# Kernel optimization log

Measured on AMD Instinct MI355X. Metric: run time of the kernel, lower is better.

Reference implementation:

```python
import jax, jax.numpy as jnp
import numpy as np

D = 1024
E = 8


def setup_inputs() -> dict:
    key = jax.random.key(0)
    ks = jax.random.split(key, 7)
    s = 1.0 / np.sqrt(D)
    x = jax.random.normal(ks[0], (4, 2048, D), dtype=jnp.float32)
    Wg = jax.random.uniform(ks[1], (D, E), minval=-s, maxval=s, dtype=jnp.float32)
    bg = jax.random.uniform(ks[2], (E,), minval=-s, maxval=s, dtype=jnp.float32)
    W1 = jax.random.uniform(ks[3], (E, D, D), minval=-s, maxval=s, dtype=jnp.float32)
    b1 = jax.random.uniform(ks[4], (E, D), minval=-s, maxval=s, dtype=jnp.float32)
    W2 = jax.random.uniform(ks[5], (E, D, D), minval=-s, maxval=s, dtype=jnp.float32)
    b2 = jax.random.uniform(ks[6], (E, D), minval=-s, maxval=s, dtype=jnp.float32)
    return {"x": x, "Wg": Wg, "bg": bg, "W1": W1, "b1": b1, "W2": W2, "b2": b2}


def reference(x, Wg, bg, W1, b1, W2, b2):
    N, T, d = x.shape
    x_flat = x.reshape(N * T, d)                                  # [NT, D]
    logits = x_flat @ Wg + bg                                     # [NT, E]
    probs = jax.nn.softmax(logits, axis=-1)
    assignments = jnp.argmax(probs, axis=-1)                      # [NT]
    # all-experts MLP (dense, as in the original module)
    h = jnp.einsum('nd,edh->neh', x_flat, W1) + b1[None]          # [NT, E, D]
    h = jax.nn.gelu(h, approximate=False)                         # torch GELU = exact erf
    eo = jnp.einsum('neh,ehd->ned', h, W2) + b2[None]             # [NT, E, D]
    selected = jnp.take_along_axis(eo, assignments[:, None, None], axis=1)[:, 0, :]  # [NT, D]
    w = jnp.take_along_axis(probs, assignments[:, None], axis=1)  # [NT, 1]
    out = (w * selected).reshape(N, T, d)
    return out
```

## Files before the change

kernel.cpp:

```cpp
#include <hip/hip_runtime.h>
#include <cstdint>

#define NT 8192
#define DD 1024
#define NE 8
#define BK 32
#define NKIT (DD / BK)
#define MAXTILE 72

typedef __attribute__((ext_vector_type(8))) _Float16 half8;
typedef __attribute__((ext_vector_type(4))) float f32x4;

__device__ __forceinline__ unsigned short f2h_bits(float f) {
  _Float16 h = (_Float16)f;
  return __builtin_bit_cast(unsigned short, h);
}

#define GLDS16(gp, lp) __builtin_amdgcn_global_load_lds( \
  (__attribute__((address_space(1))) void*)(uintptr_t)(gp), \
  (__attribute__((address_space(3))) void*)(uintptr_t)(lp), 16, 0, 0)

#define WAITCNT_VM12 0xF7C
#define WAITCNT_VM8  0xF78
#define WAITCNT_VM4  0xF74
#define WAITCNT_VM0  0xF70

__global__ __launch_bounds__(256) void wcast_kernel(
    const float* __restrict__ W1, const float* __restrict__ W2,
    _Float16* __restrict__ W1t, _Float16* __restrict__ W2t) {
  __shared__ float tile[64][65];
  const int z = blockIdx.z;
  const float* W = (z < 8 ? W1 : W2) + (size_t)(z & 7) * (DD * DD);
  _Float16* Wt   = (z < 8 ? W1t : W2t) + (size_t)(z & 7) * (DD * DD);
  const int k0 = blockIdx.x * 64, n0 = blockIdx.y * 64;
  const int tid = threadIdx.x;
#pragma unroll
  for (int it = 0; it < 4; ++it) {
    int idx = it * 256 + tid;
    int r = idx >> 4;
    int q = idx & 15;
    float4 v = *(const float4*)(W + (size_t)(k0 + r) * DD + n0 + q * 4);
    tile[r][q * 4 + 0] = v.x; tile[r][q * 4 + 1] = v.y;
    tile[r][q * 4 + 2] = v.z; tile[r][q * 4 + 3] = v.w;
  }
  __syncthreads();
#pragma unroll
  for (int it = 0; it < 4; ++it) {
    int idx = it * 256 + tid;
    int n = idx >> 4;
    int q = idx & 15;
    ushort4 o;
    o.x = f2h_bits(tile[q * 4 + 0][n]);
    o.y = f2h_bits(tile[q * 4 + 1][n]);
    o.z = f2h_bits(tile[q * 4 + 2][n]);
    o.w = f2h_bits(tile[q * 4 + 3][n]);
    *(ushort4*)(Wt + (size_t)(n0 + n) * DD + k0 + q * 4) = o;
  }
}

__global__ __launch_bounds__(256) void gate_kernel(
    const float* __restrict__ x, const float* __restrict__ Wg, const float* __restrict__ bg,
    int* __restrict__ assign, float* __restrict__ wgt, _Float16* __restrict__ xh) {
  __shared__ float WgL[NE * DD];
  const int tid = threadIdx.x;
#pragma unroll
  for (int it = 0; it < 8; ++it) {
    int idx = it * 256 + tid;
    float4 v = ((const float4*)Wg)[idx];
    int k = idx >> 1;
    int e0 = (idx & 1) * 4;
    WgL[(e0 + 0) * DD + k] = v.x;
    WgL[(e0 + 1) * DD + k] = v.y;
    WgL[(e0 + 2) * DD + k] = v.z;
    WgL[(e0 + 3) * DD + k] = v.w;
  }
  __syncthreads();
  const int lane = tid & 63, w = tid >> 6;
#pragma unroll
  for (int s = 0; s < 2; ++s) {
    const int t = blockIdx.x * 8 + w * 2 + s;
    const float4* xr = (const float4*)(x + (size_t)t * DD);
    float4 xv[4];
#pragma unroll
    for (int c = 0; c < 4; ++c) xv[c] = xr[lane + 64 * c];
    ushort4* xo = (ushort4*)(xh + (size_t)t * DD);
#pragma unroll
    for (int c = 0; c < 4; ++c) {
      union { ushort4 u; _Float16 h[4]; } cv;
      cv.h[0] = (_Float16)xv[c].x; cv.h[1] = (_Float16)xv[c].y;
      cv.h[2] = (_Float16)xv[c].z; cv.h[3] = (_Float16)xv[c].w;
      xo[lane + 64 * c] = cv.u;
    }
    float p[NE];
#pragma unroll
    for (int e = 0; e < NE; ++e) {
      float acc = 0.f;
#pragma unroll
      for (int c = 0; c < 4; ++c) {
        float4 wv = *(const float4*)&WgL[e * DD + 4 * lane + 256 * c];
        acc += xv[c].x * wv.x + xv[c].y * wv.y + xv[c].z * wv.z + xv[c].w * wv.w;
      }
      p[e] = acc;
    }
#pragma unroll
    for (int e = 0; e < NE; ++e) {
      float v = p[e];
      for (int off = 32; off > 0; off >>= 1) v += __shfl_down(v, off, 64);
      p[e] = v;
    }
    if (lane == 0) {
      float l[NE];
#pragma unroll
      for (int e = 0; e < NE; ++e) l[e] = p[e] + bg[e];
      int a = 0; float best = l[0];
#pragma unroll
      for (int e = 1; e < NE; ++e) if (l[e] > best) { best = l[e]; a = e; }
      float sum = 0.f;
#pragma unroll
      for (int e = 0; e < NE; ++e) sum += expf(l[e] - best);
      assign[t] = a;
      wgt[t] = 1.0f / sum;
    }
  }
}

__global__ __launch_bounds__(1024) void sort_kernel(
    const int* __restrict__ assign, int* __restrict__ rowtok, int* __restrict__ plan) {
  __shared__ int sc[NE * 1024];
  const int tid = threadIdx.x;
  int a[8];
  int c[NE];
#pragma unroll
  for (int e = 0; e < NE; ++e) c[e] = 0;
#pragma unroll
  for (int j = 0; j < 8; ++j) { a[j] = assign[tid * 8 + j]; ++c[a[j]]; }
#pragma unroll
  for (int e = 0; e < NE; ++e) sc[e * 1024 + tid] = c[e];
  __syncthreads();
  for (int d = 1; d < 1024; d <<= 1) {
    int add[NE];
    if (tid >= d) {
#pragma unroll
      for (int e = 0; e < NE; ++e) add[e] = sc[e * 1024 + tid - d];
    }
    __syncthreads();
    if (tid >= d) {
#pragma unroll
      for (int e = 0; e < NE; ++e) sc[e * 1024 + tid] += add[e];
    }
    __syncthreads();
  }
  int tot[NE], incl[NE];
#pragma unroll
  for (int e = 0; e < NE; ++e) { tot[e] = sc[e * 1024 + 1023]; incl[e] = sc[e * 1024 + tid]; }
  int offs[NE];
  {
    int s = 0;
#pragma unroll
    for (int e = 0; e < NE; ++e) { offs[e] = s; s += tot[e]; }
  }
  int run[NE];
#pragma unroll
  for (int e = 0; e < NE; ++e) run[e] = offs[e] + incl[e] - c[e];
#pragma unroll
  for (int j = 0; j < 8; ++j) { int e = a[j]; rowtok[run[e]++] = tid * 8 + j; }
  if (tid == 0) {
    int nt = 0;
    for (int e = 0; e < NE; ++e) {
      int cc = tot[e], st = offs[e];
      int t_cnt = (cc + 127) >> 7;
      for (int t = 0; t < t_cnt; ++t) {
        plan[1 + nt] = e;
        plan[1 + MAXTILE + nt] = st + t * 128;
        plan[1 + 2 * MAXTILE + nt] = st + cc;
        ++nt;
      }
    }
    plan[0] = nt;
  }
}

template <int MODE>
__global__ __launch_bounds__(256) void gemm_kernel(
    const _Float16* __restrict__ A,
    const _Float16* __restrict__ Wt,
    const float* __restrict__ bias,
    const int* __restrict__ plan,
    _Float16* __restrict__ Hout,
    float* __restrict__ Fout,
    const int* __restrict__ rowtok,
    const float* __restrict__ wgt) {
  const int wrk = blockIdx.x;
  const int tile = wrk >> 3;
  if (tile >= plan[0]) return;
  const int e = plan[1 + tile];
  const int m0 = plan[1 + MAXTILE + tile];
  const int seg_end = plan[1 + 2 * MAXTILE + tile];
  const int n0 = (wrk & 7) * 128;

  const int tid = threadIdx.x;
  const int lane = tid & 63;
  const int w = tid >> 6;
  const int wm = w >> 1, wn = w & 1;
  const int quad = lane >> 4;
  const int r15 = lane & 15;

  __shared__ alignas(16) _Float16 As[4 * 128 * BK];
  __shared__ alignas(16) _Float16 Bs[4 * 128 * BK];
  char* ldsA = (char*)As;
  char* ldsB = (char*)Bs;

  const _Float16* We = Wt + (size_t)e * DD * DD;
  const _Float16* gAp[2];
  const _Float16* gBp[2];
  int ldso[2];
#pragma unroll
  for (int i = 0; i < 2; ++i) {
    int slot = i * 256 + tid;
    int row = slot >> 2;
    int c = (slot & 3) ^ ((row >> 1) & 3);
    int rg = m0 + row; if (rg > NT - 1) rg = NT - 1;
    int arow = (MODE == 0) ? rowtok[rg] : rg;
    gAp[i] = A + (size_t)arow * DD + c * 8;
    gBp[i] = We + (size_t)(n0 + row) * DD + c * 8;
    ldso[i] = slot * 16;
  }

  int aoff[4], boff[4];
#pragma unroll
  for (int i = 0; i < 4; ++i) {
    int m = wm * 64 + i * 16 + r15;
    aoff[i] = m * 4 + (quad ^ ((m >> 1) & 3));
    int n = wn * 64 + i * 16 + r15;
    boff[i] = n * 4 + (quad ^ ((n >> 1) & 3));
  }

  f32x4 acc[4][4];
  f32x4 zero4 = {0.f, 0.f, 0.f, 0.f};
#pragma unroll
  for (int mi = 0; mi < 4; ++mi)
#pragma unroll
    for (int ni = 0; ni < 4; ++ni) acc[mi][ni] = zero4;

#define STAGE(KT) do {                                               \
    const int b_ = (KT) & 3;                                         \
    char* la_ = ldsA + (b_ << 13);                                   \
    char* lb_ = ldsB + (b_ << 13);                                   \
    const int ko_ = (KT) * BK;                                       \
    _Pragma("unroll") for (int i_ = 0; i_ < 2; ++i_)                 \
      GLDS16(gAp[i_] + ko_, la_ + ldso[i_]);                         \
    _Pragma("unroll") for (int i_ = 0; i_ < 2; ++i_)                 \
      GLDS16(gBp[i_] + ko_, lb_ + ldso[i_]);                         \
  } while (0)

  STAGE(0); STAGE(1); STAGE(2);

#pragma unroll 1
  for (int kt = 0; kt < NKIT; ++kt) {
    __builtin_amdgcn_s_barrier();
    __asm__ volatile("" ::: "memory");
    if (kt + 3 < NKIT) STAGE(kt + 3);
    if (kt < NKIT - 3)      __builtin_amdgcn_s_waitcnt(WAITCNT_VM12);
    else if (kt == NKIT - 3) __builtin_amdgcn_s_waitcnt(WAITCNT_VM8);
    else if (kt == NKIT - 2) __builtin_amdgcn_s_waitcnt(WAITCNT_VM4);
    else                     __builtin_amdgcn_s_waitcnt(WAITCNT_VM0);
    __builtin_amdgcn_s_barrier();
    __asm__ volatile("" ::: "memory");
    const int buf = kt & 3;
    const half8* AsV = (const half8*)(ldsA + (buf << 13));
    const half8* BsV = (const half8*)(ldsB + (buf << 13));
    half8 a[4], b[4];
#pragma unroll
    for (int i = 0; i < 4; ++i) a[i] = AsV[aoff[i]];
#pragma unroll
    for (int i = 0; i < 4; ++i) b[i] = BsV[boff[i]];
#pragma unroll
    for (int mi = 0; mi < 4; ++mi)
#pragma unroll
      for (int ni = 0; ni < 4; ++ni)
        acc[mi][ni] = __builtin_amdgcn_mfma_f32_16x16x32_f16(a[mi], b[ni], acc[mi][ni], 0, 0, 0);
  }
#undef STAGE

  const float* bptr = bias + (size_t)e * DD;
  if (MODE == 0) {
#pragma unroll
    for (int mi = 0; mi < 4; ++mi) {
      int rowb = m0 + wm * 64 + mi * 16 + quad * 4;
#pragma unroll
      for (int r = 0; r < 4; ++r) {
        int gpos = rowb + r;
        if (gpos < seg_end) {
#pragma unroll
          for (int ni = 0; ni < 4; ++ni) {
            int n = n0 + wn * 64 + ni * 16 + r15;
            float val = acc[mi][ni][r] + bptr[n];
            val = 0.5f * val * (1.0f + erff(val * 0.70710678118654752f));
            Hout[(size_t)gpos * DD + n] = (_Float16)val;
          }
        }
      }
    }
  } else {
#pragma unroll
    for (int mi = 0; mi < 4; ++mi) {
      int rowb = m0 + wm * 64 + mi * 16 + quad * 4;
#pragma unroll
      for (int r = 0; r < 4; ++r) {
        int gpos = rowb + r;
        if (gpos < seg_end) {
          int tok = rowtok[gpos];
          float wv = wgt[tok];
          float* orow = Fout + (size_t)tok * DD;
#pragma unroll
          for (int ni = 0; ni < 4; ++ni) {
            int n = n0 + wn * 64 + ni * 16 + r15;
            orow[n] = (acc[mi][ni][r] + bptr[n]) * wv;
          }
        }
      }
    }
  }
}

extern "C" void kernel_launch(void* const* d_in, const int* in_sizes, int n_in,
                              void* d_out, int out_size, void* d_ws, size_t ws_size,
                              hipStream_t stream) {
  const float* x  = (const float*)d_in[0];
  const float* Wg = (const float*)d_in[1];
  const float* bg = (const float*)d_in[2];
  const float* W1 = (const float*)d_in[3];
  const float* b1 = (const float*)d_in[4];
  const float* W2 = (const float*)d_in[5];
  const float* b2 = (const float*)d_in[6];
  float* out = (float*)d_out;

  char* ws = (char*)d_ws;
  const size_t MB16 = (size_t)1 << 24;
  _Float16* W1t = (_Float16*)(ws + 0 * MB16);
  _Float16* W2t = (_Float16*)(ws + 1 * MB16);
  _Float16* xh  = (_Float16*)(ws + 2 * MB16);
  _Float16* H   = (_Float16*)(ws + 3 * MB16);
  int*   assign = (int*)(ws + 4 * MB16);
  int*   rowtok = assign + NT;
  float* wgt    = (float*)(rowtok + NT);
  int*   plan   = (int*)(wgt + NT);

  wcast_kernel<<<dim3(16, 16, 16), 256, 0, stream>>>(W1, W2, W1t, W2t);
  gate_kernel<<<NT / 8, 256, 0, stream>>>(x, Wg, bg, assign, wgt, xh);
  sort_kernel<<<1, 1024, 0, stream>>>(assign, rowtok, plan);
  gemm_kernel<0><<<MAXTILE * 8, 256, 0, stream>>>(xh, W1t, b1, plan, H, nullptr, rowtok, nullptr);
  gemm_kernel<1><<<MAXTILE * 8, 256, 0, stream>>>(H, W2t, b2, plan, nullptr, out, rowtok, wgt);
}
```

Measured before the change: 262.5 us.

## Split GEMM K dimension across two 256-thread pipes within a block

Doubles the GEMM block to 512 threads, with each half computing the partial product over half of the K range using its own double-buffered LDS stage. The two partial accumulators are then combined through a swizzled LDS buffer before the bias, GELU or weighting epilogue. The aim is more waves per tile and more latency hiding, since only about 72x8 tiles exist and they underfill the GPU. In exchange, pipeline depth drops from four stages to two, LDS use rises to 64KB, and an extra reduction pass plus barriers is added.

```diff
diff --git a/kernel.cpp b/kernel.cpp
--- a/kernel.cpp
+++ b/kernel.cpp
@@ -5,7 +5,8 @@
 #define DD 1024
 #define NE 8
 #define BK 32
-#define NKIT (DD / BK)
+#define KHALF 512
+#define NKIT2 (KHALF / BK)
 #define MAXTILE 72
 
 typedef __attribute__((ext_vector_type(8))) _Float16 half8;
@@ -20,8 +21,6 @@
   (__attribute__((address_space(1))) void*)(uintptr_t)(gp), \
   (__attribute__((address_space(3))) void*)(uintptr_t)(lp), 16, 0, 0)
 
-#define WAITCNT_VM12 0xF7C
-#define WAITCNT_VM8  0xF78
 #define WAITCNT_VM4  0xF74
 #define WAITCNT_VM0  0xF70
 
@@ -181,7 +180,7 @@
 }
 
 template <int MODE>
-__global__ __launch_bounds__(256) void gemm_kernel(
+__global__ __launch_bounds__(512) void gemm_kernel(
     const _Float16* __restrict__ A,
     const _Float16* __restrict__ Wt,
     const float* __restrict__ bias,
@@ -199,16 +198,19 @@
   const int n0 = (wrk & 7) * 128;
 
   const int tid = threadIdx.x;
+  const int pipe = tid >> 8;
+  const int ptid = tid & 255;
   const int lane = tid & 63;
   const int w = tid >> 6;
-  const int wm = w >> 1, wn = w & 1;
+  const int pw = w & 3;
+  const int wm = pw >> 1, wn = pw & 1;
   const int quad = lane >> 4;
   const int r15 = lane & 15;
-
-  __shared__ alignas(16) _Float16 As[4 * 128 * BK];
-  __shared__ alignas(16) _Float16 Bs[4 * 128 * BK];
-  char* ldsA = (char*)As;
-  char* ldsB = (char*)Bs;
+  const int kbase = pipe * KHALF;
+
+  __shared__ alignas(16) char lds[65536];
+  char* ldsA = lds;
+  char* ldsB = lds + 32768;
 
   const _Float16* We = Wt + (size_t)e * DD * DD;
   const _Float16* gAp[2];
@@ -216,13 +218,13 @@
   int ldso[2];
 #pragma unroll
   for (int i = 0; i < 2; ++i) {
-    int slot = i * 256 + tid;
+    int slot = i * 256 + ptid;
     int row = slot >> 2;
     int c = (slot & 3) ^ ((row >> 1) & 3);
     int rg = m0 + row; if (rg > NT - 1) rg = NT - 1;
     int arow = (MODE == 0) ? rowtok[rg] : rg;
-    gAp[i] = A + (size_t)arow * DD + c * 8;
-    gBp[i] = We + (size_t)(n0 + row) * DD + c * 8;
+    gAp[i] = A + (size_t)arow * DD + kbase + c * 8;
+    gBp[i] = We + (size_t)(n0 + row) * DD + kbase + c * 8;
     ldso[i] = slot * 16;
   }
 
@@ -242,10 +244,10 @@
 #pragma unroll
     for (int ni = 0; ni < 4; ++ni) acc[mi][ni] = zero4;
 
-#define STAGE(KT) do {                                               \
-    const int b_ = (KT) & 3;                                         \
-    char* la_ = ldsA + (b_ << 13);                                   \
-    char* lb_ = ldsB + (b_ << 13);                                   \
+#define STAGE(KT, BUF) do {                                          \
+    const int rb_ = ((pipe << 1) | (BUF)) << 13;                     \
+    char* la_ = ldsA + rb_;                                          \
+    char* lb_ = ldsB + rb_;                                          \
     const int ko_ = (KT) * BK;                                       \
     _Pragma("unroll") for (int i_ = 0; i_ < 2; ++i_)                 \
       GLDS16(gAp[i_] + ko_, la_ + ldso[i_]);                         \
@@ -253,22 +255,23 @@
       GLDS16(gBp[i_] + ko_, lb_ + ldso[i_]);                         \
   } while (0)
 
-  STAGE(0); STAGE(1); STAGE(2);
+  STAGE(0, 0);
 
 #pragma unroll 1
-  for (int kt = 0; kt < NKIT; ++kt) {
+  for (int kt = 0; kt < NKIT2; ++kt) {
+    const int buf = kt & 1;
     __builtin_amdgcn_s_barrier();
     __asm__ volatile("" ::: "memory");
-    if (kt + 3 < NKIT) STAGE(kt + 3);
-    if (kt < NKIT - 3)      __builtin_amdgcn_s_waitcnt(WAITCNT_VM12);
-    else if (kt == NKIT - 3) __builtin_amdgcn_s_waitcnt(WAITCNT_VM8);
-    else if (kt == NKIT - 2) __builtin_amdgcn_s_waitcnt(WAITCNT_VM4);
-    else                     __builtin_amdgcn_s_waitcnt(WAITCNT_VM0);
+    if (kt + 1 < NKIT2) {
+      STAGE(kt + 1, buf ^ 1);
+      __builtin_amdgcn_s_waitcnt(WAITCNT_VM4);
+    } else {
+      __builtin_amdgcn_s_waitcnt(WAITCNT_VM0);
+    }
     __builtin_amdgcn_s_barrier();
     __asm__ volatile("" ::: "memory");
-    const int buf = kt & 3;
-    const half8* AsV = (const half8*)(ldsA + (buf << 13));
-    const half8* BsV = (const half8*)(ldsB + (buf << 13));
+    const half8* AsV = (const half8*)(ldsA + (((pipe << 1) | buf) << 13));
+    const half8* BsV = (const half8*)(ldsB + (((pipe << 1) | buf) << 13));
     half8 a[4], b[4];
 #pragma unroll
     for (int i = 0; i < 4; ++i) a[i] = AsV[aoff[i]];
@@ -282,40 +285,52 @@
   }
 #undef STAGE
 
+  __syncthreads();
+  float* comb = (float*)lds;
+  if (pipe == 1) {
+#pragma unroll
+    for (int mi = 0; mi < 4; ++mi) {
+      int rowb = wm * 64 + mi * 16 + quad * 4;
+#pragma unroll
+      for (int ni = 0; ni < 4; ++ni) {
+        int col = wn * 64 + ni * 16 + r15;
+        int cx = col ^ (quad << 4);
+#pragma unroll
+        for (int r = 0; r < 4; ++r) comb[(rowb + r) * 128 + cx] = acc[mi][ni][r];
+      }
+    }
+  }
+  __syncthreads();
+  if (pipe == 1) return;
+
   const float* bptr = bias + (size_t)e * DD;
-  if (MODE == 0) {
-#pragma unroll
-    for (int mi = 0; mi < 4; ++mi) {
-      int rowb = m0 + wm * 64 + mi * 16 + quad * 4;
-#pragma unroll
-      for (int r = 0; r < 4; ++r) {
-        int gpos = rowb + r;
-        if (gpos < seg_end) {
+#pragma unroll
+  for (int mi = 0; mi < 4; ++mi) {
+    int rowb = m0 + wm * 64 + mi * 16 + quad * 4;
+    int rowl = wm * 64 + mi * 16 + quad * 4;
+#pragma unroll
+    for (int r = 0; r < 4; ++r) {
+      int gpos = rowb + r;
+      if (gpos < seg_end) {
+        if (MODE == 0) {
 #pragma unroll
           for (int ni = 0; ni < 4; ++ni) {
-            int n = n0 + wn * 64 + ni * 16 + r15;
-            float val = acc[mi][ni][r] + bptr[n];
+            int col = wn * 64 + ni * 16 + r15;
+            int n = n0 + col;
+            float val = acc[mi][ni][r] + comb[(rowl + r) * 128 + (col ^ (quad << 4))] + bptr[n];
             val = 0.5f * val * (1.0f + erff(val * 0.70710678118654752f));
             Hout[(size_t)gpos * DD + n] = (_Float16)val;
           }
-        }
-      }
-    }
-  } else {
-#pragma unroll
-    for (int mi = 0; mi < 4; ++mi) {
-      int rowb = m0 + wm * 64 + mi * 16 + quad * 4;
-#pragma unroll
-      for (int r = 0; r < 4; ++r) {
-        int gpos = rowb + r;
-        if (gpos < seg_end) {
+        } else {
           int tok = rowtok[gpos];
           float wv = wgt[tok];
           float* orow = Fout + (size_t)tok * DD;
 #pragma unroll
           for (int ni = 0; ni < 4; ++ni) {
-            int n = n0 + wn * 64 + ni * 16 + r15;
-            orow[n] = (acc[mi][ni][r] + bptr[n]) * wv;
+            int col = wn * 64 + ni * 16 + r15;
+            int n = n0 + col;
+            float val = acc[mi][ni][r] + comb[(rowl + r) * 128 + (col ^ (quad << 4))] + bptr[n];
+            orow[n] = val * wv;
           }
         }
       }
@@ -349,6 +364,6 @@
   wcast_kernel<<<dim3(16, 16, 16), 256, 0, stream>>>(W1, W2, W1t, W2t);
   gate_kernel<<<NT / 8, 256, 0, stream>>>(x, Wg, bg, assign, wgt, xh);
   sort_kernel<<<1, 1024, 0, stream>>>(assign, rowtok, plan);
-  gemm_kernel<0><<<MAXTILE * 8, 256, 0, stream>>>(xh, W1t, b1, plan, H, nullptr, rowtok, nullptr);
-  gemm_kernel<1><<<MAXTILE * 8, 256, 0, stream>>>(H, W2t, b2, plan, nullptr, out, rowtok, wgt);
-}
+  gemm_kernel<0><<<MAXTILE * 8, 512, 0, stream>>>(xh, W1t, b1, plan, H, nullptr, rowtok, nullptr);
+  gemm_kernel<1><<<MAXTILE * 8, 512, 0, stream>>>(H, W2t, b2, plan, nullptr, out, rowtok, wgt);
+}
```

Result: no change. 263.7 us (+0.4%).

## Shrink GEMM tile to 64x128 and switch to double-buffered LDS pipeline

Applied to the files above, without the earlier changes.

Grouped expert GEMM tiles change from 128x128 to 64x128 rows, with each of the four waves covering all 64 rows and a 32-column slice. MAXTILE is raised to match. The 4-stage global-to-LDS prefetch becomes a 2-stage double buffer, cutting LDS from 64KB to 24KB. This aims to reduce padding waste on partially filled expert segments, launch more blocks, and raise occupancy. The cost is less arithmetic per loaded byte and a shallower prefetch that may hide memory latency less well. The launch grid must also be sized for the larger tile count, and that code is not visible here.

```diff
diff --git a/kernel.cpp b/kernel.cpp
--- a/kernel.cpp
+++ b/kernel.cpp
@@ -6,7 +6,8 @@
 #define NE 8
 #define BK 32
 #define NKIT (DD / BK)
-#define MAXTILE 72
+#define TM 64
+#define MAXTILE 136
 
 typedef __attribute__((ext_vector_type(8))) _Float16 half8;
 typedef __attribute__((ext_vector_type(4))) float f32x4;
@@ -20,9 +21,7 @@
   (__attribute__((address_space(1))) void*)(uintptr_t)(gp), \
   (__attribute__((address_space(3))) void*)(uintptr_t)(lp), 16, 0, 0)
 
-#define WAITCNT_VM12 0xF7C
-#define WAITCNT_VM8  0xF78
-#define WAITCNT_VM4  0xF74
+#define WAITCNT_VM3  0xF73
 #define WAITCNT_VM0  0xF70
 
 __global__ __launch_bounds__(256) void wcast_kernel(
@@ -168,10 +167,10 @@
     int nt = 0;
     for (int e = 0; e < NE; ++e) {
       int cc = tot[e], st = offs[e];
-      int t_cnt = (cc + 127) >> 7;
+      int t_cnt = (cc + TM - 1) / TM;
       for (int t = 0; t < t_cnt; ++t) {
         plan[1 + nt] = e;
-        plan[1 + MAXTILE + nt] = st + t * 128;
+        plan[1 + MAXTILE + nt] = st + t * TM;
         plan[1 + 2 * MAXTILE + nt] = st + cc;
         ++nt;
       }
@@ -200,121 +199,117 @@
 
   const int tid = threadIdx.x;
   const int lane = tid & 63;
-  const int w = tid >> 6;
-  const int wm = w >> 1, wn = w & 1;
+  const int wn = tid >> 6;
   const int quad = lane >> 4;
   const int r15 = lane & 15;
 
-  __shared__ alignas(16) _Float16 As[4 * 128 * BK];
-  __shared__ alignas(16) _Float16 Bs[4 * 128 * BK];
-  char* ldsA = (char*)As;
-  char* ldsB = (char*)Bs;
+  __shared__ alignas(16) char lds[24576];
+  char* ldsA = lds;
+  char* ldsB = lds + 8192;
 
   const _Float16* We = Wt + (size_t)e * DD * DD;
-  const _Float16* gAp[2];
+  const _Float16* gAp;
   const _Float16* gBp[2];
-  int ldso[2];
+  int ldsoA, ldsoB[2];
+  {
+    int slot = tid;
+    int row = slot >> 2;
+    int c = (slot & 3) ^ ((row >> 1) & 3);
+    int rg = m0 + row; if (rg > NT - 1) rg = NT - 1;
+    int arow = (MODE == 0) ? rowtok[rg] : rg;
+    gAp = A + (size_t)arow * DD + c * 8;
+    ldsoA = slot * 16;
+  }
 #pragma unroll
   for (int i = 0; i < 2; ++i) {
     int slot = i * 256 + tid;
     int row = slot >> 2;
     int c = (slot & 3) ^ ((row >> 1) & 3);
-    int rg = m0 + row; if (rg > NT - 1) rg = NT - 1;
-    int arow = (MODE == 0) ? rowtok[rg] : rg;
-    gAp[i] = A + (size_t)arow * DD + c * 8;
     gBp[i] = We + (size_t)(n0 + row) * DD + c * 8;
-    ldso[i] = slot * 16;
-  }
-
-  int aoff[4], boff[4];
+    ldsoB[i] = slot * 16;
+  }
+
+  int aoff[4], boff[2];
 #pragma unroll
   for (int i = 0; i < 4; ++i) {
-    int m = wm * 64 + i * 16 + r15;
+    int m = i * 16 + r15;
     aoff[i] = m * 4 + (quad ^ ((m >> 1) & 3));
-    int n = wn * 64 + i * 16 + r15;
+  }
+#pragma unroll
+  for (int i = 0; i < 2; ++i) {
+    int n = wn * 32 + i * 16 + r15;
     boff[i] = n * 4 + (quad ^ ((n >> 1) & 3));
   }
 
-  f32x4 acc[4][4];
+  f32x4 acc[4][2];
   f32x4 zero4 = {0.f, 0.f, 0.f, 0.f};
 #pragma unroll
   for (int mi = 0; mi < 4; ++mi)
 #pragma unroll
-    for (int ni = 0; ni < 4; ++ni) acc[mi][ni] = zero4;
-
-#define STAGE(KT) do {                                               \
-    const int b_ = (KT) & 3;                                         \
-    char* la_ = ldsA + (b_ << 13);                                   \
-    char* lb_ = ldsB + (b_ << 13);                                   \
+    for (int ni = 0; ni < 2; ++ni) acc[mi][ni] = zero4;
+
+#define STAGE(KT, BUF) do {                                          \
     const int ko_ = (KT) * BK;                                       \
-    _Pragma("unroll") for (int i_ = 0; i_ < 2; ++i_)                 \
-      GLDS16(gAp[i_] + ko_, la_ + ldso[i_]);                         \
-    _Pragma("unroll") for (int i_ = 0; i_ < 2; ++i_)                 \
-      GLDS16(gBp[i_] + ko_, lb_ + ldso[i_]);                         \
+    char* la_ = ldsA + ((BUF) << 12);                                \
+    char* lb_ = ldsB + ((BUF) << 13);                                \
+    GLDS16(gAp + ko_, la_ + ldsoA);                                  \
+    GLDS16(gBp[0] + ko_, lb_ + ldsoB[0]);                            \
+    GLDS16(gBp[1] + ko_, lb_ + ldsoB[1]);                            \
   } while (0)
 
-  STAGE(0); STAGE(1); STAGE(2);
+  STAGE(0, 0);
 
 #pragma unroll 1
   for (int kt = 0; kt < NKIT; ++kt) {
+    const int buf = kt & 1;
     __builtin_amdgcn_s_barrier();
     __asm__ volatile("" ::: "memory");
-    if (kt + 3 < NKIT) STAGE(kt + 3);
-    if (kt < NKIT - 3)      __builtin_amdgcn_s_waitcnt(WAITCNT_VM12);
-    else if (kt == NKIT - 3) __builtin_amdgcn_s_waitcnt(WAITCNT_VM8);
-    else if (kt == NKIT - 2) __builtin_amdgcn_s_waitcnt(WAITCNT_VM4);
-    else                     __builtin_amdgcn_s_waitcnt(WAITCNT_VM0);
+    if (kt + 1 < NKIT) {
+      STAGE(kt + 1, buf ^ 1);
+      __builtin_amdgcn_s_waitcnt(WAITCNT_VM3);
+    } else {
+      __builtin_amdgcn_s_waitcnt(WAITCNT_VM0);
+    }
     __builtin_amdgcn_s_barrier();
     __asm__ volatile("" ::: "memory");
-    const int buf = kt & 3;
-    const half8* AsV = (const half8*)(ldsA + (buf << 13));
+    const half8* AsV = (const half8*)(ldsA + (buf << 12));
     const half8* BsV = (const half8*)(ldsB + (buf << 13));
-    half8 a[4], b[4];
+    half8 a[4], b[2];
 #pragma unroll
     for (int i = 0; i < 4; ++i) a[i] = AsV[aoff[i]];
 #pragma unroll
-    for (int i = 0; i < 4; ++i) b[i] = BsV[boff[i]];
+    for (int i = 0; i < 2; ++i) b[i] = BsV[boff[i]];
 #pragma unroll
     for (int mi = 0; mi < 4; ++mi)
 #pragma unroll
-      for (int ni = 0; ni < 4; ++ni)
+      for (int ni = 0; ni < 2; ++ni)
         acc[mi][ni] = __builtin_amdgcn_mfma_f32_16x16x32_f16(a[mi], b[ni], acc[mi][ni], 0, 0, 0);
   }
 #undef STAGE
 
   const float* bptr = bias + (size_t)e * DD;
-  if (MODE == 0) {
-#pragma unroll
-    for (int mi = 0; mi < 4; ++mi) {
-      int rowb = m0 + wm * 64 + mi * 16 + quad * 4;
-#pragma unroll
-      for (int r = 0; r < 4; ++r) {
-        int gpos = rowb + r;
-        if (gpos < seg_end) {
-#pragma unroll
-          for (int ni = 0; ni < 4; ++ni) {
-            int n = n0 + wn * 64 + ni * 16 + r15;
+#pragma unroll
+  for (int mi = 0; mi < 4; ++mi) {
+    int rowb = m0 + mi * 16 + quad * 4;
+#pragma unroll
+    for (int r = 0; r < 4; ++r) {
+      int gpos = rowb + r;
+      if (gpos < seg_end) {
+        if (MODE == 0) {
+#pragma unroll
+          for (int ni = 0; ni < 2; ++ni) {
+            int n = n0 + wn * 32 + ni * 16 + r15;
             float val = acc[mi][ni][r] + bptr[n];
             val = 0.5f * val * (1.0f + erff(val * 0.70710678118654752f));
             Hout[(size_t)gpos * DD + n] = (_Float16)val;
           }
-        }
-      }
-    }
-  } else {
-#pragma unroll
-    for (int mi = 0; mi < 4; ++mi) {
-      int rowb = m0 + wm * 64 + mi * 16 + quad * 4;
-#pragma unroll
-      for (int r = 0; r < 4; ++r) {
-        int gpos = rowb + r;
-        if (gpos < seg_end) {
+        } else {
           int tok = rowtok[gpos];
           float wv = wgt[tok];
           float* orow = Fout + (size_t)tok * DD;
 #pragma unroll
-          for (int ni = 0; ni < 4; ++ni) {
-            int n = n0 + wn * 64 + ni * 16 + r15;
+          for (int ni = 0; ni < 2; ++ni) {
+            int n = n0 + wn * 32 + ni * 16 + r15;
             orow[n] = (acc[mi][ni][r] + bptr[n]) * wv;
           }
         }
```

Result: faster. 254.9 us (-2.9%).
